# Kernel tuning notes

Hardware: AMD Instinct MI355X
Metric: run time of the kernel (lower is better)

## Reference

```python
import jax, jax.numpy as jnp
import numpy as np

# Architecture constants (from init_kwargs / ActionConfig)
R = 4          # vae_time_compression_ratio
WS = 2         # windows_size
PAD_T = R * WS # preprocessor left-padding
HID = 512      # action hidden_size
KD_IN = 16     # keyboard_dim_in (movement feature dim)
C_IMG = 3072   # img_hidden_size
KH = 1024      # keyboard_hidden_dim
NH = 16        # heads_num
HD = 64        # keyboard_head_dim
EPS = 1e-6


def setup_inputs() -> dict:
    key = jax.random.key(0)
    ks = jax.random.split(key, 8)
    B, T, Hs, Ws, NF = 1, 3, 44, 80, 81
    S = Hs * Ws

    def w(k, shape, s=0.02):
        return jax.random.normal(k, shape, jnp.float32) * s

    return {
        "x": jax.random.normal(ks[0], (B, T * S, C_IMG), jnp.float32),
        "condition": jax.random.normal(ks[1], (B, NF, KD_IN), jnp.float32),
        "me_w1": w(ks[2], (KD_IN, HID)), "me_b1": jnp.zeros((HID,), jnp.float32),
        "me_w2": w(ks[3], (HID, HID)), "me_b2": jnp.zeros((HID,), jnp.float32),
        "q_w": w(ks[4], (C_IMG, KH)), "q_b": jnp.zeros((KH,), jnp.float32),
        "kv_w": w(ks[5], (HID * WS * R, 2 * KH)), "kv_b": jnp.zeros((2 * KH,), jnp.float32),
        "qn_w": jnp.ones((HD,), jnp.float32), "kn_w": jnp.ones((HD,), jnp.float32),
        "out_w": w(ks[6], (KH, C_IMG)), "out_b": jnp.zeros((C_IMG,), jnp.float32),
        "H": Hs, "W": Ws, "T": T, "num_frame_per_block": T,
    }


def _rmsnorm(x, w):
    return x * jax.lax.rsqrt(jnp.mean(x * x, axis=-1, keepdims=True) + EPS) * w


def _preprocess(condition, me_w1, me_b1, me_w2, me_b2, num_frame_per_block):
    # MovementPreprocessor.forward with is_causal=True
    B, NF, _ = condition.shape
    pad = jnp.broadcast_to(condition[:, :1, :], (B, PAD_T, condition.shape[-1]))
    cp = jnp.concatenate([pad, condition], axis=1)            # [B, PAD_T+NF, KD_IN]
    emb = jax.nn.silu(cp @ me_w1 + me_b1) @ me_w2 + me_b2     # [B, PAD_T+NF, HID]
    n_feats = (NF - 1) // R + 1
    start = R * (n_feats - num_frame_per_block - WS) + PAD_T  # python int (static)
    emb = emb[:, start:, :]
    # vectorized replacement of the python-loop window slicing+stack
    win = jnp.arange(num_frame_per_block)[:, None] * R + jnp.arange(WS * R)[None, :]
    gm = emb[:, win, :]                                       # [B, L, WS*R, HID]
    return gm.reshape(B, num_frame_per_block, WS * R * HID)   # [B, L, 4096]


def reference(x, condition, me_w1, me_b1, me_w2, me_b2, q_w, q_b, kv_w, kv_b,
              qn_w, kn_w, out_w, out_b, H, W, T, num_frame_per_block):
    B = x.shape[0]
    S = H * W
    L = num_frame_per_block

    mf = _preprocess(condition, me_w1, me_b1, me_w2, me_b2, L)  # [B, L, HID*WS*R]

    # q: [B, T*S, C_IMG] -> [B, S, T, h, d]
    q = (x @ q_w + q_b).reshape(B, T, S, NH, HD).transpose(0, 2, 1, 3, 4)

    # k, v: [B, L, h, d] (NOT expanded over S; broadcast inside attention instead)
    kv = (mf @ kv_w + kv_b).reshape(B, L, 2, NH, HD)
    k, v = kv[:, :, 0], kv[:, :, 1]

    q = _rmsnorm(q, qn_w)
    k = _rmsnorm(k, kn_w)

    scale = 1.0 / np.sqrt(HD).astype(np.float32)
    scores = jnp.einsum('bsthd,blhd->bshtl', q, k) * scale      # [B,S,h,T,L]
    attn = jax.nn.softmax(scores, axis=-1)
    o = jnp.einsum('bshtl,blhd->bsthd', attn, v)                # [B,S,T,h,d]

    # '(B S) T H D -> B (T S) (H D)'
    o = o.transpose(0, 2, 1, 3, 4).reshape(B, T * S, NH * HD)
    return x + (o @ out_w + out_b)
```

## Files before the change

kernel.cpp:

```cpp
#include <hip/hip_runtime.h>

#define TOK  10560
#define CIMG 3072
#define KHD  1024

typedef unsigned short ushort_t;
typedef unsigned int u32;
using bf16x8 = __attribute__((ext_vector_type(8))) __bf16;
using f32x4  = __attribute__((ext_vector_type(4))) float;

#define GLD_LDS16(gp, lp) __builtin_amdgcn_global_load_lds( \
    (const __attribute__((address_space(1))) u32*)(gp), \
    (__attribute__((address_space(3))) u32*)(lp), 16, 0, 0)

static __device__ __forceinline__ unsigned short f2bf(float f){
  union { float f; unsigned u; } x; x.f = f;
  unsigned r = x.u + 0x7fffu + ((x.u >> 16) & 1u);
  return (unsigned short)(r >> 16);
}
static __device__ __forceinline__ float wave_sum(float v){
  #pragma unroll
  for (int off = 32; off > 0; off >>= 1) v += __shfl_xor(v, off, 64);
  return v;
}

__global__ __launch_bounds__(256) void k_pre1(const float* __restrict__ cond,
    const float* __restrict__ w1, const float* __restrict__ b1,
    float* __restrict__ h1){
  __shared__ float cs[16][16];
  int t = threadIdx.x;
  if (t < 256) cs[t >> 4][t & 15] = cond[(64 + (t >> 4)) * 16 + (t & 15)];
  __syncthreads();
  #pragma unroll
  for (int i = 0; i < 4; ++i){
    int idx = blockIdx.x * 256 + t + i * 2048;
    int r = idx >> 9, c = idx & 511;
    float s = b1[c];
    #pragma unroll
    for (int j = 0; j < 16; ++j) s += cs[r][j] * w1[j * 512 + c];
    h1[idx] = s / (1.f + __expf(-s));
  }
}

__global__ __launch_bounds__(256) void k_pre2(const float* __restrict__ h1,
    const float* __restrict__ w2, const float* __restrict__ b2,
    float* __restrict__ emb){
  int idx = blockIdx.x * 256 + threadIdx.x;
  int r = idx >> 9, c = idx & 511;
  const float* hp = h1 + r * 512;
  const float* wp = w2 + c;
  float acc = b2[c];
  #pragma unroll 8
  for (int j = 0; j < 512; ++j) acc += hp[j] * wp[(size_t)j * 512];
  emb[idx] = acc;
}

__global__ __launch_bounds__(256) void k_kv(const float* __restrict__ emb,
                                            const float* __restrict__ kvw,
                                            float* __restrict__ part){
  int bl = blockIdx.x;
  int l = bl / 128, rem = bl % 128, nt = rem / 16, kc = rem % 16;
  int n = nt * 256 + threadIdx.x;
  const float* e = emb + 2048 * l + kc * 256;
  const float* w = kvw + (size_t)(kc * 256) * 2048 + n;
  float acc = 0.f;
  for (int r = 0; r < 256; ++r) acc += e[r] * w[(size_t)r * 2048];
  part[kc * 6144 + l * 2048 + n] = acc;
}

__global__ void k_knorm(const float* __restrict__ part, const float* __restrict__ kvb,
                        const float* __restrict__ knw, float* __restrict__ kn,
                        float* __restrict__ vv){
  int wid = threadIdx.x >> 6, lane = threadIdx.x & 63;
  for (int i = 0; i < 12; ++i){
    int g = wid * 12 + i;
    int l = g >> 4, h = g & 15;
    int ik = l * 2048 + h * 64 + lane;
    float kk = kvb[h * 64 + lane];
    float v  = kvb[1024 + h * 64 + lane];
    for (int p = 0; p < 16; ++p){ kk += part[p * 6144 + ik]; v += part[p * 6144 + ik + 1024]; }
    float ss = wave_sum(kk * kk);
    kn[l * 1024 + h * 64 + lane] = kk * rsqrtf(ss * (1.f/64.f) + 1e-6f) * knw[lane];
    vv[l * 1024 + h * 64 + lane] = v;
  }
}

__global__ __launch_bounds__(256) void k_tconv(const float* __restrict__ src,
                                               ushort_t* __restrict__ dst,
                                               int R, int C){
  __shared__ float tile[32][33];
  int nTr = R >> 5;
  int tr = blockIdx.x % nTr, tc = blockIdx.x / nTr;
  int r0 = tr * 32, c0 = tc * 32, t = threadIdx.x;
  #pragma unroll
  for (int i = 0; i < 4; ++i){
    int idx = t + i * 256; int r = idx >> 5, c = idx & 31;
    tile[r][c] = src[(size_t)(r0 + r) * C + c0 + c];
  }
  __syncthreads();
  #pragma unroll
  for (int i = 0; i < 4; ++i){
    int idx = t + i * 256; int rr = idx >> 5, cc = idx & 31;
    dst[(size_t)(c0 + rr) * R + r0 + cc] = f2bf(tile[cc][rr]);
  }
}

__global__ __launch_bounds__(256) void k_xconv(const float* __restrict__ x,
                                               ushort_t* __restrict__ xb, int n4){
  for (int i = blockIdx.x * 256 + threadIdx.x; i < n4; i += gridDim.x * 256){
    float4 v = ((const float4*)x)[i];
    ushort4 o;
    o.x = f2bf(v.x); o.y = f2bf(v.y); o.z = f2bf(v.z); o.w = f2bf(v.w);
    ((ushort4*)xb)[i] = o;
  }
}

__global__ __launch_bounds__(512, 4) void gemm_fused(
    const ushort_t* __restrict__ A, const ushort_t* __restrict__ Bt,
    const float* __restrict__ bias, const float* __restrict__ kn,
    const float* __restrict__ qnw, float* __restrict__ acoef){
  __shared__ __align__(16) unsigned char lds[81920];
  const int tid = threadIdx.x;
  const int lane = tid & 63, wid = tid >> 6;
  const int wm = wid >> 1, wn = wid & 1;
  const int l15 = lane & 15, kg = lane >> 4;

  int bid = blockIdx.x;
  bid = (bid & 7) * 55 + (bid >> 3);
  const int mt = bid >> 3, nt = bid & 7;
  const int mbase = mt * 192, nbase = nt << 7;

  const int sr  = tid >> 1;
  const int skh = (tid & 1) ^ ((sr >> 2) & 1);
  const ushort_t* gA = A + (size_t)(mbase + sr) * CIMG + skh * 8;
  const int u   = tid - 384;
  const int skb = (u & 1) ^ ((u >> 3) & 1);
  const ushort_t* gB0 = Bt + (size_t)(nbase + (u >> 1)) * CIMG + skb * 8;
  const ushort_t* gB1 = gB0 + (size_t)64 * CIMG;

  auto stage = [&](int t, int c, int b){
    const int gk = t * 64 + c * 16;
    if (wid < 6){
      unsigned char* dst = lds + b * 40960 + c * 6144 + wid * 1024;
      GLD_LDS16(gA + gk, dst);
    } else {
      unsigned char* dst = lds + b * 40960 + 24576 + c * 4096 + (wid - 6) * 1024;
      GLD_LDS16(gB0 + gk, dst);
      GLD_LDS16(gB1 + gk, dst + 2048);
    }
  };
#define WAITC2 { if (wid < 6) asm volatile("s_waitcnt vmcnt(2)" ::: "memory"); \
                 else         asm volatile("s_waitcnt vmcnt(4)" ::: "memory"); }

  const int arl = wm * 48 + l15;
  const int brl = wn * 64 + l15;
  const int kh  = ((kg & 1) ^ ((l15 >> 2) & 1)) * 16;
  const unsigned aBase = (unsigned)((kg >> 1) * 6144 + arl * 32 + kh);
  const unsigned bBase = (unsigned)(24576 + (kg >> 1) * 4096 + brl * 32 + kh);

  f32x4 acc[3][4];
  #pragma unroll
  for (int m = 0; m < 3; ++m)
    #pragma unroll
    for (int n = 0; n < 4; ++n) acc[m][n] = {0.f, 0.f, 0.f, 0.f};

  bf16x8 afr[3], bfr[4];

#define PH_READ(base, KSL) { _Pragma("unroll") \
    for (int n = 0; n < 4; ++n) \
      bfr[n] = *(const bf16x8*)((base) + bBase + (KSL)*8192 + n*512); \
    _Pragma("unroll") \
    for (int m = 0; m < 3; ++m) \
      afr[m] = *(const bf16x8*)((base) + aBase + (KSL)*12288 + m*512); }
#define PH_MFMA { __builtin_amdgcn_s_setprio(1); _Pragma("unroll") \
    for (int m = 0; m < 3; ++m){ _Pragma("unroll") \
      for (int n = 0; n < 4; ++n) \
        acc[m][n] = __builtin_amdgcn_mfma_f32_16x16x32_bf16(afr[m], bfr[n], acc[m][n], 0, 0, 0); } \
    __builtin_amdgcn_s_setprio(0); }

  const int T = CIMG / 64;

  stage(0, 0, 0); stage(0, 1, 0); stage(0, 2, 0); stage(0, 3, 0);
  WAITC2;
  __builtin_amdgcn_s_barrier();

  for (int t = 0; t < T - 1; ++t){
    const int b = t & 1;
    const unsigned char* base = lds + b * 40960;
    PH_READ(base, 0);
    stage(t + 1, 0, b ^ 1); stage(t + 1, 1, b ^ 1);
    WAITC2;
    __builtin_amdgcn_s_barrier();
    PH_MFMA;
    __builtin_amdgcn_s_barrier();
    PH_READ(base, 1);
    stage(t + 1, 2, b ^ 1); stage(t + 1, 3, b ^ 1);
    WAITC2;
    __builtin_amdgcn_s_barrier();
    PH_MFMA;
    __builtin_amdgcn_s_barrier();
  }
  {
    const unsigned char* base = lds + ((T - 1) & 1) * 40960;
    PH_READ(base, 0);
    asm volatile("s_waitcnt vmcnt(0)" ::: "memory");
    __builtin_amdgcn_s_barrier();
    PH_MFMA;
    __builtin_amdgcn_s_barrier();
    PH_READ(base, 1);
    PH_MFMA;
  }
#undef PH_READ
#undef PH_MFMA
#undef WAITC2

  const int hglob = nt * 2 + wn;
  float qnwv[4], qbv[4], knv0[4], knv1[4], knv2[4];
  #pragma unroll
  for (int n = 0; n < 4; ++n){
    int d = n * 16 + l15;
    qnwv[n] = qnw[d];
    qbv[n]  = bias[nbase + wn * 64 + d];
    knv0[n] = kn[hglob * 64 + d];
    knv1[n] = kn[1024 + hglob * 64 + d];
    knv2[n] = kn[2048 + hglob * 64 + d];
  }
  #pragma unroll
  for (int m = 0; m < 3; ++m){
    #pragma unroll
    for (int j = 0; j < 4; ++j){
      float q[4], ssq = 0.f;
      #pragma unroll
      for (int n = 0; n < 4; ++n){ q[n] = acc[m][n][j] + qbv[n]; ssq += q[n] * q[n]; }
      #pragma unroll
      for (int off = 1; off < 16; off <<= 1) ssq += __shfl_xor(ssq, off, 64);
      float rs = rsqrtf(ssq * (1.f/64.f) + 1e-6f);
      float s0 = 0.f, s1 = 0.f, s2 = 0.f;
      #pragma unroll
      for (int n = 0; n < 4; ++n){
        float qn = q[n] * rs * qnwv[n];
        s0 += qn * knv0[n]; s1 += qn * knv1[n]; s2 += qn * knv2[n];
      }
      #pragma unroll
      for (int off = 1; off < 16; off <<= 1){
        s0 += __shfl_xor(s0, off, 64);
        s1 += __shfl_xor(s1, off, 64);
        s2 += __shfl_xor(s2, off, 64);
      }
      s0 *= 0.125f; s1 *= 0.125f; s2 *= 0.125f;
      float mx = fmaxf(s0, fmaxf(s1, s2));
      float e0 = __expf(s0 - mx), e1 = __expf(s1 - mx), e2 = __expf(s2 - mx);
      float inv = 1.f / (e0 + e1 + e2);
      int grow = mbase + wm * 48 + m * 16 + kg * 4 + j;
      if (l15 == 0){
        float2 a12 = {e1 * inv, e2 * inv};
        *(float2*)(acoef + (size_t)grow * 32 + hglob * 2) = a12;
      }
    }
  }
}

__global__ __launch_bounds__(512) void k_uv(const float* __restrict__ vv,
    const float* __restrict__ ow, float* __restrict__ U){
  int b = blockIdx.x;
  int i = b / 6, cc = b % 6;
  int h = i / 3, l = i % 3;
  int c = cc * 512 + threadIdx.x;
  const float* vp = vv + l * 1024 + h * 64;
  const float* wp = ow + (size_t)(h * 64) * 3072 + c;
  float acc = 0.f;
  #pragma unroll
  for (int d = 0; d < 64; ++d) acc += vp[d] * wp[(size_t)d * 3072];
  U[(size_t)i * 3072 + c] = acc;
}

__global__ __launch_bounds__(256) void k_ubase(const float* __restrict__ U,
    const float* __restrict__ ob, float* __restrict__ base, float* __restrict__ D){
  int c = blockIdx.x * 256 + threadIdx.x;
  float b = ob[c];
  #pragma unroll
  for (int h = 0; h < 16; ++h){
    float u0 = U[(size_t)(h * 3 + 0) * 3072 + c];
    float u1 = U[(size_t)(h * 3 + 1) * 3072 + c];
    float u2 = U[(size_t)(h * 3 + 2) * 3072 + c];
    b += u0;
    D[(size_t)(h * 2 + 0) * 3072 + c] = u1 - u0;
    D[(size_t)(h * 2 + 1) * 3072 + c] = u2 - u0;
  }
  base[c] = b;
}

__global__ __launch_bounds__(256) void k_rank32v(const float* __restrict__ x,
    const float* __restrict__ acoef, const float* __restrict__ D,
    const float* __restrict__ base, float* __restrict__ out){
  __shared__ __align__(16) float as[8][32];
  const int tid = threadIdx.x;
  const int rb = blockIdx.x / 3, cc = blockIdx.x % 3;
  const int r0 = rb * 8;
  const int c  = cc * 1024 + tid * 4;

  f32x4 xv[8];
  #pragma unroll
  for (int r = 0; r < 8; ++r)
    xv[r] = *(const f32x4*)(x + (size_t)(r0 + r) * 3072 + c);

  if (tid < 256) ((float*)as)[tid] = acoef[(size_t)r0 * 32 + tid];
  __syncthreads();

  f32x4 accv[8];
  #pragma unroll
  for (int r = 0; r < 8; ++r) accv[r] = {0.f, 0.f, 0.f, 0.f};

  #pragma unroll
  for (int k4 = 0; k4 < 8; ++k4){
    f32x4 d0 = *(const f32x4*)(D + (size_t)(k4 * 4 + 0) * 3072 + c);
    f32x4 d1 = *(const f32x4*)(D + (size_t)(k4 * 4 + 1) * 3072 + c);
    f32x4 d2 = *(const f32x4*)(D + (size_t)(k4 * 4 + 2) * 3072 + c);
    f32x4 d3 = *(const f32x4*)(D + (size_t)(k4 * 4 + 3) * 3072 + c);
    #pragma unroll
    for (int r = 0; r < 8; ++r){
      f32x4 a4 = *(const f32x4*)(&as[r][k4 * 4]);
      accv[r][0] += a4[0]*d0[0] + a4[1]*d1[0] + a4[2]*d2[0] + a4[3]*d3[0];
      accv[r][1] += a4[0]*d0[1] + a4[1]*d1[1] + a4[2]*d2[1] + a4[3]*d3[1];
      accv[r][2] += a4[0]*d0[2] + a4[1]*d1[2] + a4[2]*d2[2] + a4[3]*d3[2];
      accv[r][3] += a4[0]*d0[3] + a4[1]*d1[3] + a4[2]*d2[3] + a4[3]*d3[3];
    }
  }

  f32x4 b4 = *(const f32x4*)(base + c);
  #pragma unroll
  for (int r = 0; r < 8; ++r){
    const size_t o = (size_t)(r0 + r) * 3072 + c;
    f32x4 ov;
    ov[0] = xv[r][0] + b4[0] + accv[r][0];
    ov[1] = xv[r][1] + b4[1] + accv[r][1];
    ov[2] = xv[r][2] + b4[2] + accv[r][2];
    ov[3] = xv[r][3] + b4[3] + accv[r][3];
    *(f32x4*)(out + o) = ov;
  }
}

extern "C" void kernel_launch(void* const* d_in, const int* in_sizes, int n_in,
                              void* d_out, int out_size, void* d_ws, size_t ws_size,
                              hipStream_t stream){
  const float* x    = (const float*)d_in[0];
  const float* cond = (const float*)d_in[1];
  const float* mew1 = (const float*)d_in[2];
  const float* meb1 = (const float*)d_in[3];
  const float* mew2 = (const float*)d_in[4];
  const float* meb2 = (const float*)d_in[5];
  const float* qw   = (const float*)d_in[6];
  const float* qb   = (const float*)d_in[7];
  const float* kvw  = (const float*)d_in[8];
  const float* kvb  = (const float*)d_in[9];
  const float* qnw  = (const float*)d_in[10];
  const float* knw  = (const float*)d_in[11];
  const float* ow   = (const float*)d_in[12];
  const float* ob   = (const float*)d_in[13];

  char* ws = (char*)d_ws;
  float*    emb    = (float*)(ws + 0);
  float*    kvpart = (float*)(ws + 32768);
  float*    kn     = (float*)(ws + 425984);
  float*    vv     = (float*)(ws + 438272);
  ushort_t* qwt    = (ushort_t*)(ws + 450560);
  float*    U      = (float*)(ws + 6742016);
  float*    base   = (float*)(ws + 7331840);
  float*    Dbuf   = (float*)(ws + 7344128);
  float*    acoef  = (float*)(ws + 7737344);
  float*    h1buf  = (float*)(ws + 9089024);

  ushort_t* xb = (ushort_t*)d_out;

  k_pre1<<<8, 256, 0, stream>>>(cond, mew1, meb1, h1buf);
  k_pre2<<<32, 256, 0, stream>>>(h1buf, mew2, meb2, emb);
  k_kv<<<384, 256, 0, stream>>>(emb, kvw, kvpart);
  k_knorm<<<1, 256, 0, stream>>>(kvpart, kvb, knw, kn, vv);
  k_uv<<<288, 512, 0, stream>>>(vv, ow, U);
  k_ubase<<<12, 256, 0, stream>>>(U, ob, base, Dbuf);
  k_tconv<<<3072, 256, 0, stream>>>(qw, qwt, 3072, 1024);
  k_xconv<<<2048, 256, 0, stream>>>(x, xb, (TOK * CIMG) / 4);
  gemm_fused<<<440, 512, 0, stream>>>(xb, qwt, qb, kn, qnw, acoef);
  k_rank32v<<<3960, 256, 0, stream>>>(x, acoef, Dbuf, base, (float*)d_out);
}
```

Measured before the change: 281.5 us.

## Fuse preprocessor MLP and U/D kernels, simplify GEMM pipeline to one barrier per tile

Merges k_pre1 and k_pre2 into a single kernel that keeps the SiLU hidden layer in shared memory, with each of the 32 blocks recomputing the first layer. Merges k_uv and k_ubase into one k_uvd kernel that computes the three value projections per head and writes base/D directly, dropping the U buffer and two launches. The main GEMM's K-loop changes from half-tile staging with partial vmcnt waits and four barriers per tile to loading a whole tile ahead with one full wait and one barrier. Fewer launches and barriers come at the cost of less parallelism in k_uvd (only 6 blocks) and possibly less memory/compute overlap in the GEMM, since each tile now waits with vmcnt(0).

```diff
diff --git a/kernel.cpp b/kernel.cpp
--- a/kernel.cpp
+++ b/kernel.cpp
@@ -24,34 +24,31 @@
   return v;
 }
 
-__global__ __launch_bounds__(256) void k_pre1(const float* __restrict__ cond,
+__global__ __launch_bounds__(256) void k_pre(const float* __restrict__ cond,
     const float* __restrict__ w1, const float* __restrict__ b1,
-    float* __restrict__ h1){
+    const float* __restrict__ w2, const float* __restrict__ b2,
+    float* __restrict__ emb){
   __shared__ float cs[16][16];
+  __shared__ float h1[16][512];
   int t = threadIdx.x;
   if (t < 256) cs[t >> 4][t & 15] = cond[(64 + (t >> 4)) * 16 + (t & 15)];
   __syncthreads();
   #pragma unroll
-  for (int i = 0; i < 4; ++i){
-    int idx = blockIdx.x * 256 + t + i * 2048;
+  for (int i = 0; i < 32; ++i){
+    int idx = t + i * 256;
     int r = idx >> 9, c = idx & 511;
     float s = b1[c];
     #pragma unroll
     for (int j = 0; j < 16; ++j) s += cs[r][j] * w1[j * 512 + c];
-    h1[idx] = s / (1.f + __expf(-s));
-  }
-}
-
-__global__ __launch_bounds__(256) void k_pre2(const float* __restrict__ h1,
-    const float* __restrict__ w2, const float* __restrict__ b2,
-    float* __restrict__ emb){
-  int idx = blockIdx.x * 256 + threadIdx.x;
+    h1[r][c] = s / (1.f + __expf(-s));
+  }
+  __syncthreads();
+  int idx = blockIdx.x * 256 + t;
   int r = idx >> 9, c = idx & 511;
-  const float* hp = h1 + r * 512;
-  const float* wp = w2 + c;
+  const float* hp = h1[r];
   float acc = b2[c];
   #pragma unroll 8
-  for (int j = 0; j < 512; ++j) acc += hp[j] * wp[(size_t)j * 512];
+  for (int j = 0; j < 512; ++j) acc += hp[j] * w2[(size_t)j * 512 + c];
   emb[idx] = acc;
 }
 
@@ -85,6 +82,27 @@
   }
 }
 
+__global__ __launch_bounds__(512) void k_uvd(const float* __restrict__ vv,
+    const float* __restrict__ ow, const float* __restrict__ ob,
+    float* __restrict__ base, float* __restrict__ D){
+  int c = blockIdx.x * 512 + threadIdx.x;
+  float bacc = ob[c];
+  for (int h = 0; h < 16; ++h){
+    float u0 = 0.f, u1 = 0.f, u2 = 0.f;
+    const float* wp = ow + (size_t)(h * 64) * 3072 + c;
+    const float* vp = vv + h * 64;
+    #pragma unroll 8
+    for (int d = 0; d < 64; ++d){
+      float w = wp[(size_t)d * 3072];
+      u0 += vp[d] * w; u1 += vp[1024 + d] * w; u2 += vp[2048 + d] * w;
+    }
+    bacc += u0;
+    D[(size_t)(h * 2 + 0) * 3072 + c] = u1 - u0;
+    D[(size_t)(h * 2 + 1) * 3072 + c] = u2 - u0;
+  }
+  base[c] = bacc;
+}
+
 __global__ __launch_bounds__(256) void k_tconv(const float* __restrict__ src,
                                                ushort_t* __restrict__ dst,
                                                int R, int C){
@@ -138,19 +156,21 @@
   const ushort_t* gB0 = Bt + (size_t)(nbase + (u >> 1)) * CIMG + skb * 8;
   const ushort_t* gB1 = gB0 + (size_t)64 * CIMG;
 
-  auto stage = [&](int t, int c, int b){
-    const int gk = t * 64 + c * 16;
+  auto stage = [&](int t, int b){
+    const int gk = t * 64;
     if (wid < 6){
-      unsigned char* dst = lds + b * 40960 + c * 6144 + wid * 1024;
-      GLD_LDS16(gA + gk, dst);
+      #pragma unroll
+      for (int c = 0; c < 4; ++c)
+        GLD_LDS16(gA + gk + c * 16, lds + b * 40960 + c * 6144 + wid * 1024);
     } else {
-      unsigned char* dst = lds + b * 40960 + 24576 + c * 4096 + (wid - 6) * 1024;
-      GLD_LDS16(gB0 + gk, dst);
-      GLD_LDS16(gB1 + gk, dst + 2048);
+      #pragma unroll
+      for (int c = 0; c < 4; ++c){
+        unsigned char* dst = lds + b * 40960 + 24576 + c * 4096 + (wid - 6) * 1024;
+        GLD_LDS16(gB0 + gk + c * 16, dst);
+        GLD_LDS16(gB1 + gk + c * 16, dst + 2048);
+      }
     }
   };
-#define WAITC2 { if (wid < 6) asm volatile("s_waitcnt vmcnt(2)" ::: "memory"); \
-                 else         asm volatile("s_waitcnt vmcnt(4)" ::: "memory"); }
 
   const int arl = wm * 48 + l15;
   const int brl = wn * 64 + l15;
@@ -180,39 +200,21 @@
 
   const int T = CIMG / 64;
 
-  stage(0, 0, 0); stage(0, 1, 0); stage(0, 2, 0); stage(0, 3, 0);
-  WAITC2;
-  __builtin_amdgcn_s_barrier();
-
-  for (int t = 0; t < T - 1; ++t){
-    const int b = t & 1;
-    const unsigned char* base = lds + b * 40960;
-    PH_READ(base, 0);
-    stage(t + 1, 0, b ^ 1); stage(t + 1, 1, b ^ 1);
-    WAITC2;
-    __builtin_amdgcn_s_barrier();
-    PH_MFMA;
-    __builtin_amdgcn_s_barrier();
-    PH_READ(base, 1);
-    stage(t + 1, 2, b ^ 1); stage(t + 1, 3, b ^ 1);
-    WAITC2;
-    __builtin_amdgcn_s_barrier();
-    PH_MFMA;
-    __builtin_amdgcn_s_barrier();
-  }
-  {
-    const unsigned char* base = lds + ((T - 1) & 1) * 40960;
-    PH_READ(base, 0);
+  stage(0, 0);
+
+  for (int t = 0; t < T; ++t){
+    const unsigned char* base = lds + (t & 1) * 40960;
     asm volatile("s_waitcnt vmcnt(0)" ::: "memory");
     __builtin_amdgcn_s_barrier();
+    asm volatile("" ::: "memory");
+    PH_READ(base, 0);
+    if (t + 1 < T) stage(t + 1, (t + 1) & 1);
     PH_MFMA;
-    __builtin_amdgcn_s_barrier();
     PH_READ(base, 1);
     PH_MFMA;
   }
 #undef PH_READ
 #undef PH_MFMA
-#undef WAITC2
 
   const int hglob = nt * 2 + wn;
   float qnwv[4], qbv[4], knv0[4], knv1[4], knv2[4];
@@ -258,36 +260,6 @@
       }
     }
   }
-}
-
-__global__ __launch_bounds__(512) void k_uv(const float* __restrict__ vv,
-    const float* __restrict__ ow, float* __restrict__ U){
-  int b = blockIdx.x;
-  int i = b / 6, cc = b % 6;
-  int h = i / 3, l = i % 3;
-  int c = cc * 512 + threadIdx.x;
-  const float* vp = vv + l * 1024 + h * 64;
-  const float* wp = ow + (size_t)(h * 64) * 3072 + c;
-  float acc = 0.f;
-  #pragma unroll
-  for (int d = 0; d < 64; ++d) acc += vp[d] * wp[(size_t)d * 3072];
-  U[(size_t)i * 3072 + c] = acc;
-}
-
-__global__ __launch_bounds__(256) void k_ubase(const float* __restrict__ U,
-    const float* __restrict__ ob, float* __restrict__ base, float* __restrict__ D){
-  int c = blockIdx.x * 256 + threadIdx.x;
-  float b = ob[c];
-  #pragma unroll
-  for (int h = 0; h < 16; ++h){
-    float u0 = U[(size_t)(h * 3 + 0) * 3072 + c];
-    float u1 = U[(size_t)(h * 3 + 1) * 3072 + c];
-    float u2 = U[(size_t)(h * 3 + 2) * 3072 + c];
-    b += u0;
-    D[(size_t)(h * 2 + 0) * 3072 + c] = u1 - u0;
-    D[(size_t)(h * 2 + 1) * 3072 + c] = u2 - u0;
-  }
-  base[c] = b;
 }
 
 __global__ __launch_bounds__(256) void k_rank32v(const float* __restrict__ x,
@@ -364,20 +336,16 @@
   float*    kn     = (float*)(ws + 425984);
   float*    vv     = (float*)(ws + 438272);
   ushort_t* qwt    = (ushort_t*)(ws + 450560);
-  float*    U      = (float*)(ws + 6742016);
   float*    base   = (float*)(ws + 7331840);
   float*    Dbuf   = (float*)(ws + 7344128);
   float*    acoef  = (float*)(ws + 7737344);
-  float*    h1buf  = (float*)(ws + 9089024);
 
   ushort_t* xb = (ushort_t*)d_out;
 
-  k_pre1<<<8, 256, 0, stream>>>(cond, mew1, meb1, h1buf);
-  k_pre2<<<32, 256, 0, stream>>>(h1buf, mew2, meb2, emb);
+  k_pre<<<32, 256, 0, stream>>>(cond, mew1, meb1, mew2, meb2, emb);
   k_kv<<<384, 256, 0, stream>>>(emb, kvw, kvpart);
   k_knorm<<<1, 256, 0, stream>>>(kvpart, kvb, knw, kn, vv);
-  k_uv<<<288, 512, 0, stream>>>(vv, ow, U);
-  k_ubase<<<12, 256, 0, stream>>>(U, ob, base, Dbuf);
+  k_uvd<<<6, 512, 0, stream>>>(vv, ow, ob, base, Dbuf);
   k_tconv<<<3072, 256, 0, stream>>>(qw, qwt, 3072, 1024);
   k_xconv<<<2048, 256, 0, stream>>>(x, xb, (TOK * CIMG) / 4);
   gemm_fused<<<440, 512, 0, stream>>>(xb, qwt, qb, kn, qnw, acoef);
```

Result: slower. 384.5 us (+36.6%).
